# Performance work log

Measured on AMD Instinct MI355X. Metric: run time of the kernel, lower is better.

The kernel has to match this reference:

```python
import jax, jax.numpy as jnp
import numpy as np

B, S, T = 1024, 1024, 32  # batch, seq_len, num_tags


def setup_inputs() -> dict:
    key = jax.random.key(0)
    k1, k2, k3, k4 = jax.random.split(key, 4)
    logits = jax.random.normal(k1, (B, S, T), dtype=jnp.float32)
    transitions = jax.random.normal(k2, (T, T), dtype=jnp.float32)
    tags = jax.random.randint(k3, (B, S), 0, T)
    lengths = jax.random.randint(k4, (B,), 1, S + 1)
    return {"logits": logits, "transitions": transitions, "tags": tags, "lengths": lengths}


def _forward_alg(logits, transitions):
    # viterbi_0 = logits[:, 0, :]; then for t>=1:
    # v_next[b, j] = logsumexp_i(v[b, i] + trans[i, j]) + logits[b, t, j]
    v0 = logits[:, 0, :]  # (B, T)
    emits = jnp.swapaxes(logits[:, 1:, :], 0, 1)  # (S-1, B, T)

    def step(v, emit_t):
        v_next = jax.nn.logsumexp(v[:, :, None] + transitions[None, :, :], axis=1) + emit_t
        return v_next, None

    v_final, _ = jax.lax.scan(step, v0, emits)
    return jax.nn.logsumexp(v_final, axis=1)  # (B,)


def _score_sentence(logits, transitions, tags, lengths):
    # emission scores of gold tags, masked to t < length (note: original ignores
    # lengths in the forward algorithm but uses them here, faithfully reproduced)
    emit = jnp.take_along_axis(logits, tags[:, :, None], axis=2)[..., 0]  # (B, S)
    pos = jnp.arange(S)
    emit_mask = (pos[None, :] < lengths[:, None]).astype(logits.dtype)
    score = jnp.sum(emit * emit_mask, axis=1)
    # transition scores trans[tags[t-1], tags[t]] for 1 <= t < length
    trans_sc = transitions[tags[:, :-1], tags[:, 1:]]  # (B, S-1)
    trans_mask = (pos[None, 1:] < lengths[:, None]).astype(logits.dtype)
    score = score + jnp.sum(trans_sc * trans_mask, axis=1)
    return score  # (B,)


def reference(logits, transitions, tags, lengths):
    log_z = _forward_alg(logits, transitions)
    gold = _score_sentence(logits, transitions, tags, lengths)
    return jnp.mean(log_z - gold)
```

## Files before the change

### kernel.cpp

```cpp
#include <hip/hip_runtime.h>

#define NB 1024
#define NS 1024
#define NT 32
#define L2E 1.44269504088896340736f
#define LN2 0.69314718055994530942f

typedef short        bfrag  __attribute__((ext_vector_type(8)));
typedef float        cfrag  __attribute__((ext_vector_type(16)));
typedef __bf16       bf16x2 __attribute__((ext_vector_type(2)));
typedef float        f32x8  __attribute__((ext_vector_type(8)));
typedef float        f32x4  __attribute__((ext_vector_type(4)));
typedef float        f32x2  __attribute__((ext_vector_type(2)));
typedef unsigned int u32;
typedef unsigned int u32x4  __attribute__((ext_vector_type(4)));

__device__ __forceinline__ float fexp2(float x){ return __builtin_amdgcn_exp2f(x); }
__device__ __forceinline__ float flog2(float x){ return __builtin_amdgcn_logf(x); }

__device__ __forceinline__ u32 pkbf_rne(float a, float b){
    f32x2 t; t.x = a; t.y = b;
    return __builtin_bit_cast(u32, __builtin_convertvector(t, bf16x2));
}
__device__ __forceinline__ u32 pkbf_t(float a, float b){
    return __builtin_amdgcn_perm(__builtin_bit_cast(u32, b),
                                 __builtin_bit_cast(u32, a), 0x07060302u);
}
__device__ __forceinline__ bfrag mk_afrag(f32x8 v){
    u32x4 r;
    r[0] = pkbf_rne(v[0], v[1]); r[1] = pkbf_rne(v[2], v[3]);
    r[2] = pkbf_rne(v[4], v[5]); r[3] = pkbf_rne(v[6], v[7]);
    return __builtin_bit_cast(bfrag, r);
}
__device__ __forceinline__ int exref(float ref){
    u32 xb = __builtin_bit_cast(u32, ref);
    u32 xf = __builtin_amdgcn_readfirstlane(xb);
    int ex = (int)((xf >> 23) & 0xFFu) - 127;
    return ex < -120 ? -120 : (ex > 120 ? 120 : ex);
}

__device__ __forceinline__ int rho(int k){
    int bb = (k >> 2) & 3;
    return (bb == 1 || bb == 2) ? (k ^ 12) : k;
}

template<int N> struct ic { static constexpr int value = N; };
union accu { cfrag c; f32x2 p[8]; };
union q4u  { f32x4 v; f32x2 p[2]; };

__global__ __launch_bounds__(256, 8) void crf_chunk(
    const float* __restrict__ logits, const float* __restrict__ trans,
    const int* __restrict__ tags, const int* __restrict__ lens,
    u32* __restrict__ wmat, float* __restrict__ woff,
    float* __restrict__ gpart, float* __restrict__ outz)
{
    __shared__ __align__(16) float dscall[4 * 512];

    const int tid = threadIdx.x;
    const int wv  = tid >> 6, lt = tid & 63;
    const int m   = lt & 31,  h  = lt >> 5;
    const int bc  = blockIdx.x * 4 + wv;
    const int b   = bc >> 3,  c  = bc & 7;
    float* dsc = dscall + wv * 512;

    if (blockIdx.x == 0 && tid == 0) *outz = 0.0f;

    const float* base = logits + (size_t)b * NS * NT;
    const int    len  = lens[b];
    const int    tb   = b * NS;

    f32x8 Et0, Et1;
    #pragma unroll
    for (int j = 0; j < 8; j++){
        Et0[j] = fexp2(L2E * trans[rho(     8*h + j)*NT + m]);
        Et1[j] = fexp2(L2E * trans[rho(16 + 8*h + j)*NT + m]);
    }
    const bfrag A0f = mk_afrag(Et0);
    const bfrag A1f = mk_afrag(Et1);

    u32x4 B0v, B1v;
    #pragma unroll
    for (int d = 0; d < 4; d++){
        int k0 = 8*h + 2*d;      u32 v = 0;
        if (rho(k0)     == m) v |= 0x3F80u;
        if (rho(k0 + 1) == m) v |= 0x3F800000u;
        B0v[d] = v;
        int k1 = 16 + 8*h + 2*d; v = 0;
        if (rho(k1)     == m) v |= 0x3F80u;
        if (rho(k1 + 1) == m) v |= 0x3F800000u;
        B1v[d] = v;
    }

    cfrag zacc;
    #pragma unroll
    for (int q = 0; q < 16; q++) zacc[q] = 0.0f;

    int   offi = 0;
    float exf  = 0.0f;
    const int tbeg = c*128 + 1;

    float eA[4], eB[4];

    auto issue = [&](float (&e)[4], int k){
        const int t0 = tbeg + k*8 + 4*h;
        #pragma unroll
        for (int i = 0; i < 4; i++){
            int t = t0 + i; t = t > (NS-1) ? (NS-1) : t;
            e[i] = base[t*NT + m];
        }
    };
    auto commit = [&](float (&e)[4], int k){
        float* sp = dsc + (k & 1)*256 + (4*h)*32 + m;
        float a0 = (h == 0) ? -exf : 0.0f;
        sp[0]    = fexp2(fmaf(L2E, e[0], a0));
        sp[32]   = fexp2(L2E * e[1]);
        sp[64]   = fexp2(L2E * e[2]);
        sp[96]   = fexp2(L2E * e[3]);
    };

    auto procN = [&](int k, bool defer, auto nstc){
        constexpr int NST = decltype(nstc)::value;
        const float* db = dsc + (k & 1)*256 + 4*h;
        #pragma unroll
        for (int i = 0; i < NST; i++){
            accu acc;
            acc.c = __builtin_amdgcn_mfma_f32_32x32x16_bf16(
                        A0f, __builtin_bit_cast(bfrag, B0v), zacc, 0, 0, 0);
            acc.c = __builtin_amdgcn_mfma_f32_32x32x16_bf16(
                        A1f, __builtin_bit_cast(bfrag, B1v), acc.c, 0, 0, 0);

            q4u d0, d1, d2, d3;
            d0.v = *(const f32x4*)(db + i*32 +  0);
            d1.v = *(const f32x4*)(db + i*32 +  8);
            d2.v = *(const f32x4*)(db + i*32 + 16);
            d3.v = *(const f32x4*)(db + i*32 + 24);
            acc.p[0] *= d0.p[0]; acc.p[1] *= d0.p[1];
            acc.p[2] *= d1.p[0]; acc.p[3] *= d1.p[1];
            acc.p[4] *= d2.p[0]; acc.p[5] *= d2.p[1];
            acc.p[6] *= d3.p[0]; acc.p[7] *= d3.p[1];

            if (i == 3){
                int ex = exref(fmaxf(acc.c[0], acc.c[8]));
                offi += ex;
                f32x2 s2;
                s2.x = s2.y = __builtin_bit_cast(float, (u32)(127 - ex) << 23);
                #pragma unroll
                for (int q = 0; q < 8; q++) acc.p[q] *= s2;
            }
            if (i == 7 && defer){
                int ex = exref(fmaxf(acc.c[0], acc.c[8]));
                offi += ex;
                exf = (float)ex;
            }

            B0v[0] = pkbf_t(acc.c[0],  acc.c[1]);  B0v[1] = pkbf_t(acc.c[2],  acc.c[3]);
            B0v[2] = pkbf_t(acc.c[4],  acc.c[5]);  B0v[3] = pkbf_t(acc.c[6],  acc.c[7]);
            B1v[0] = pkbf_t(acc.c[8],  acc.c[9]);  B1v[1] = pkbf_t(acc.c[10], acc.c[11]);
            B1v[2] = pkbf_t(acc.c[12], acc.c[13]); B1v[3] = pkbf_t(acc.c[14], acc.c[15]);
        }
    };

    issue(eA, 0); commit(eA, 0);
    #pragma unroll 1
    for (int k = 0; k < 14; k += 2){
        issue(eB, k + 1);
        procN(k, true, ic<8>{});
        commit(eB, k + 1);
        issue(eA, k + 2);
        procN(k + 1, true, ic<8>{});
        commit(eA, k + 2);
    }
    issue(eB, 15);
    procN(14, true, ic<8>{});
    commit(eB, 15);
    if (c != 7) procN(15, false, ic<8>{});
    else        procN(15, false, ic<7>{});

    {
        u32* wp = wmat + (size_t)bc * 512 + (size_t)lt * 8;
        *(u32x4*)(wp)     = B0v;
        *(u32x4*)(wp + 4) = B1v;
    }
    if (lt == 0) woff[bc] = (float)offi;

    {
        const int t1 = tbeg + 2*lt;
        const int t2 = t1 + 1;
        const int i2 = t2 > (NS-1) ? (NS-1) : t2;
        const int g0 = tags[tb + t1 - 1];
        const int g1 = tags[tb + t1];
        const int g2 = tags[tb + i2];
        float gg = 0.0f;
        if (t1 < len) gg += base[t1*NT + g1] + trans[g0*NT + g1];
        if (t2 < len) gg += base[t2*NT + g2] + trans[g1*NT + g2];
        #pragma unroll
        for (int d = 1; d < 64; d <<= 1) gg += __shfl_xor(gg, d, 64);
        if (lt == 0){
            if (c == 0) gg += base[tags[tb]];
            gpart[bc] = gg;
        }
    }
}

__global__ __launch_bounds__(256) void crf_combine(
    const float* __restrict__ logits,
    const u32* __restrict__ wmat, const float* __restrict__ woff,
    const float* __restrict__ gpart, float* __restrict__ out)
{
    const int tid = threadIdx.x;
    const int wv  = tid >> 6, lt = tid & 63;
    const int m   = lt & 31,  h  = lt >> 5;
    const int b   = blockIdx.x * 4 + wv;
    const float* base = logits + (size_t)b * NS * NT;

    uint4 mf[16];
    const u32* wb = wmat + (size_t)b * 8 * 512 + (size_t)lt * 8;
    #pragma unroll
    for (int j = 0; j < 8; j++){
        mf[2*j]     = *(const uint4*)(wb + j*512);
        mf[2*j + 1] = *(const uint4*)(wb + j*512 + 4);
    }

    float4 gp0 = ((const float4*)(gpart + b*8))[0];
    float4 gp1 = ((const float4*)(gpart + b*8))[1];
    const float gold = (gp0.x + gp0.y) + (gp0.z + gp0.w)
                     + (gp1.x + gp1.y) + (gp1.z + gp1.w);

    float voff = 0.0f;
    #pragma unroll
    for (int cc = 0; cc < 8; cc++) voff += woff[b*8 + cc];

    u32x4 S0, S1;
    #pragma unroll
    for (int d = 0; d < 4; d++){
        int k0 = 8*h + 2*d;      u32 v = 0;
        if (rho(k0)     == m) v |= 0x3F80u;
        if (rho(k0 + 1) == m) v |= 0x3F800000u;
        S0[d] = v;
        int k1 = 16 + 8*h + 2*d; v = 0;
        if (rho(k1)     == m) v |= 0x3F80u;
        if (rho(k1 + 1) == m) v |= 0x3F800000u;
        S1[d] = v;
    }

    cfrag zacc;
    #pragma unroll
    for (int q = 0; q < 16; q++) zacc[q] = 0.0f;

    #pragma unroll
    for (int j = 7; j >= 0; j--){
        accu acc;
        acc.c = __builtin_amdgcn_mfma_f32_32x32x16_bf16(
                    __builtin_bit_cast(bfrag, mf[2*j]),
                    __builtin_bit_cast(bfrag, S0), zacc, 0, 0, 0);
        acc.c = __builtin_amdgcn_mfma_f32_32x32x16_bf16(
                    __builtin_bit_cast(bfrag, mf[2*j + 1]),
                    __builtin_bit_cast(bfrag, S1), acc.c, 0, 0, 0);

        float mx = acc.c[0];
        #pragma unroll
        for (int q = 1; q < 16; q++) mx = fmaxf(mx, acc.c[q]);
        #pragma unroll
        for (int d = 1; d < 64; d <<= 1) mx = fmaxf(mx, __shfl_xor(mx, d, 64));
        int ex = exref(mx);
        float sc = __builtin_bit_cast(float, (u32)(127 - ex) << 23);
        #pragma unroll
        for (int q = 0; q < 16; q++) acc.c[q] *= sc;
        voff += (float)ex;

        S0[0] = pkbf_t(acc.c[0],  acc.c[1]);  S0[1] = pkbf_t(acc.c[2],  acc.c[3]);
        S0[2] = pkbf_t(acc.c[4],  acc.c[5]);  S0[3] = pkbf_t(acc.c[6],  acc.c[7]);
        S1[0] = pkbf_t(acc.c[8],  acc.c[9]);  S1[1] = pkbf_t(acc.c[10], acc.c[11]);
        S1[2] = pkbf_t(acc.c[12], acc.c[13]); S1[3] = pkbf_t(acc.c[14], acc.c[15]);
    }

    u32x4 V0, V1;
    #pragma unroll
    for (int d = 0; d < 4; d++){
        int k0 = 8*h + 2*d;
        V0[d] = pkbf_rne(fexp2(L2E * base[rho(k0)]), fexp2(L2E * base[rho(k0+1)]));
        int k1 = 16 + 8*h + 2*d;
        V1[d] = pkbf_rne(fexp2(L2E * base[rho(k1)]), fexp2(L2E * base[rho(k1+1)]));
    }

    accu fin;
    fin.c = __builtin_amdgcn_mfma_f32_32x32x16_bf16(
                __builtin_bit_cast(bfrag, S0), __builtin_bit_cast(bfrag, V0),
                zacc, 0, 0, 0);
    fin.c = __builtin_amdgcn_mfma_f32_32x32x16_bf16(
                __builtin_bit_cast(bfrag, S1), __builtin_bit_cast(bfrag, V1),
                fin.c, 0, 0, 0);

    float s = 0.0f;
    #pragma unroll
    for (int q = 0; q < 16; q++) s += fin.c[q];
    s += __shfl_xor(s, 32, 64);

    if (lt == 0){
        float logz = LN2 * (voff + flog2(s));
        atomicAdd(out, (logz - gold) * (1.0f / (float)NB));
    }
}

extern "C" void kernel_launch(void* const* d_in, const int* in_sizes, int n_in,
                              void* d_out, int out_size, void* d_ws, size_t ws_size,
                              hipStream_t stream) {
    const float* logits = (const float*)d_in[0];
    const float* trans  = (const float*)d_in[1];
    const int*   tags   = (const int*)d_in[2];
    const int*   lens   = (const int*)d_in[3];

    u32*   wmat  = (u32*)d_ws;
    float* woff  = (float*)((char*)d_ws + 16u*1024u*1024u);
    float* gpart = woff + 8192;

    crf_chunk  <<<2048, 256, 0, stream>>>(logits, trans, tags, lens,
                                          wmat, woff, gpart, (float*)d_out);
    crf_combine<<< 256, 256, 0, stream>>>(logits, wmat, woff, gpart,
                                          (float*)d_out);
}
```

Before: 248.5 us.

## Split each wave's 128-step chunk into two interleaved 64-step sub-chains

Each wave now runs two independent transfer-matrix chains over the low and high halves of its 128-step chunk. Their MFMAs are interleaved so one chain's dependency latency is hidden behind the other's work, and the two products are merged at the end with two extra MFMA pairs and a rescale. This shortens the serial MFMA dependency chain per wave. The cost is doubled LDS per wave and more registers, so launch bounds drop from 8 to 4 blocks per SM, which lowers occupancy.

```diff
diff --git a/kernel.cpp b/kernel.cpp
--- a/kernel.cpp
+++ b/kernel.cpp
@@ -48,20 +48,24 @@
 union accu { cfrag c; f32x2 p[8]; };
 union q4u  { f32x4 v; f32x2 p[2]; };
 
-__global__ __launch_bounds__(256, 8) void crf_chunk(
+#define MFMA(A,B,C) __builtin_amdgcn_mfma_f32_32x32x16_bf16( \
+    (A), __builtin_bit_cast(bfrag, B), (C), 0, 0, 0)
+
+__global__ __launch_bounds__(256, 4) void crf_chunk(
     const float* __restrict__ logits, const float* __restrict__ trans,
     const int* __restrict__ tags, const int* __restrict__ lens,
     u32* __restrict__ wmat, float* __restrict__ woff,
     float* __restrict__ gpart, float* __restrict__ outz)
 {
-    __shared__ __align__(16) float dscall[4 * 512];
+    __shared__ __align__(16) float dscall[4 * 1024];
 
     const int tid = threadIdx.x;
     const int wv  = tid >> 6, lt = tid & 63;
     const int m   = lt & 31,  h  = lt >> 5;
     const int bc  = blockIdx.x * 4 + wv;
     const int b   = bc >> 3,  c  = bc & 7;
-    float* dsc = dscall + wv * 512;
+    float* dscL = dscall + wv * 1024;
+    float* dscH = dscL + 512;
 
     if (blockIdx.x == 0 && tid == 0) *outz = 0.0f;
 
@@ -78,30 +82,34 @@
     const bfrag A0f = mk_afrag(Et0);
     const bfrag A1f = mk_afrag(Et1);
 
-    u32x4 B0v, B1v;
+    u32x4 I0, I1;
     #pragma unroll
     for (int d = 0; d < 4; d++){
         int k0 = 8*h + 2*d;      u32 v = 0;
         if (rho(k0)     == m) v |= 0x3F80u;
         if (rho(k0 + 1) == m) v |= 0x3F800000u;
-        B0v[d] = v;
+        I0[d] = v;
         int k1 = 16 + 8*h + 2*d; v = 0;
         if (rho(k1)     == m) v |= 0x3F80u;
         if (rho(k1 + 1) == m) v |= 0x3F800000u;
-        B1v[d] = v;
-    }
+        I1[d] = v;
+    }
+
+    u32x4 L0 = I0, L1 = I1;
+    u32x4 H0 = I0, H1 = I1;
 
     cfrag zacc;
     #pragma unroll
     for (int q = 0; q < 16; q++) zacc[q] = 0.0f;
 
-    int   offi = 0;
-    float exf  = 0.0f;
-    const int tbeg = c*128 + 1;
-
-    float eA[4], eB[4];
-
-    auto issue = [&](float (&e)[4], int k){
+    int   offiL = 0,    offiH = 0;
+    float exfL  = 0.0f, exfH  = 0.0f;
+    const int tbegL = c*128 + 1;
+    const int tbegH = c*128 + 65;
+
+    float eLA[4], eLB[4], eHA[4], eHB[4];
+
+    auto issue = [&](float (&e)[4], int k, int tbeg){
         const int t0 = tbeg + k*8 + 4*h;
         #pragma unroll
         for (int i = 0; i < 4; i++){
@@ -109,7 +117,7 @@
             e[i] = base[t*NT + m];
         }
     };
-    auto commit = [&](float (&e)[4], int k){
+    auto commit = [&](float (&e)[4], int k, float* dsc, float exf){
         float* sp = dsc + (k & 1)*256 + (4*h)*32 + m;
         float a0 = (h == 0) ? -exf : 0.0f;
         sp[0]    = fexp2(fmaf(L2E, e[0], a0));
@@ -118,73 +126,134 @@
         sp[96]   = fexp2(L2E * e[3]);
     };
 
-    auto procN = [&](int k, bool defer, auto nstc){
-        constexpr int NST = decltype(nstc)::value;
-        const float* db = dsc + (k & 1)*256 + 4*h;
-        #pragma unroll
-        for (int i = 0; i < NST; i++){
-            accu acc;
-            acc.c = __builtin_amdgcn_mfma_f32_32x32x16_bf16(
-                        A0f, __builtin_bit_cast(bfrag, B0v), zacc, 0, 0, 0);
-            acc.c = __builtin_amdgcn_mfma_f32_32x32x16_bf16(
-                        A1f, __builtin_bit_cast(bfrag, B1v), acc.c, 0, 0, 0);
-
-            q4u d0, d1, d2, d3;
-            d0.v = *(const f32x4*)(db + i*32 +  0);
-            d1.v = *(const f32x4*)(db + i*32 +  8);
-            d2.v = *(const f32x4*)(db + i*32 + 16);
-            d3.v = *(const f32x4*)(db + i*32 + 24);
-            acc.p[0] *= d0.p[0]; acc.p[1] *= d0.p[1];
-            acc.p[2] *= d1.p[0]; acc.p[3] *= d1.p[1];
-            acc.p[4] *= d2.p[0]; acc.p[5] *= d2.p[1];
-            acc.p[6] *= d3.p[0]; acc.p[7] *= d3.p[1];
+    auto proc2 = [&](int k, bool defer, auto nhC){
+        constexpr int NH = decltype(nhC)::value;
+        const float* dbL = dscL + (k & 1)*256 + 4*h;
+        const float* dbH = dscH + (k & 1)*256 + 4*h;
+        #pragma unroll
+        for (int i = 0; i < 8; i++){
+            accu aL, aH;
+            aL.c = MFMA(A0f, L0, zacc);
+            if (i < NH) aH.c = MFMA(A0f, H0, zacc);
+            aL.c = MFMA(A1f, L1, aL.c);
+            if (i < NH) aH.c = MFMA(A1f, H1, aH.c);
+
+            {
+                q4u d0, d1, d2, d3;
+                d0.v = *(const f32x4*)(dbL + i*32 +  0);
+                d1.v = *(const f32x4*)(dbL + i*32 +  8);
+                d2.v = *(const f32x4*)(dbL + i*32 + 16);
+                d3.v = *(const f32x4*)(dbL + i*32 + 24);
+                aL.p[0] *= d0.p[0]; aL.p[1] *= d0.p[1];
+                aL.p[2] *= d1.p[0]; aL.p[3] *= d1.p[1];
+                aL.p[4] *= d2.p[0]; aL.p[5] *= d2.p[1];
+                aL.p[6] *= d3.p[0]; aL.p[7] *= d3.p[1];
+            }
+            if (i < NH){
+                q4u d0, d1, d2, d3;
+                d0.v = *(const f32x4*)(dbH + i*32 +  0);
+                d1.v = *(const f32x4*)(dbH + i*32 +  8);
+                d2.v = *(const f32x4*)(dbH + i*32 + 16);
+                d3.v = *(const f32x4*)(dbH + i*32 + 24);
+                aH.p[0] *= d0.p[0]; aH.p[1] *= d0.p[1];
+                aH.p[2] *= d1.p[0]; aH.p[3] *= d1.p[1];
+                aH.p[4] *= d2.p[0]; aH.p[5] *= d2.p[1];
+                aH.p[6] *= d3.p[0]; aH.p[7] *= d3.p[1];
+            }
 
             if (i == 3){
-                int ex = exref(fmaxf(acc.c[0], acc.c[8]));
-                offi += ex;
-                f32x2 s2;
-                s2.x = s2.y = __builtin_bit_cast(float, (u32)(127 - ex) << 23);
+                int exL = exref(fmaxf(aL.c[0], aL.c[8]));
+                offiL += exL;
+                f32x2 s2; s2.x = s2.y =
+                    __builtin_bit_cast(float, (u32)(127 - exL) << 23);
                 #pragma unroll
-                for (int q = 0; q < 8; q++) acc.p[q] *= s2;
+                for (int q = 0; q < 8; q++) aL.p[q] *= s2;
+                int exH = exref(fmaxf(aH.c[0], aH.c[8]));
+                offiH += exH;
+                f32x2 s3; s3.x = s3.y =
+                    __builtin_bit_cast(float, (u32)(127 - exH) << 23);
+                #pragma unroll
+                for (int q = 0; q < 8; q++) aH.p[q] *= s3;
             }
             if (i == 7 && defer){
-                int ex = exref(fmaxf(acc.c[0], acc.c[8]));
-                offi += ex;
-                exf = (float)ex;
-            }
-
-            B0v[0] = pkbf_t(acc.c[0],  acc.c[1]);  B0v[1] = pkbf_t(acc.c[2],  acc.c[3]);
-            B0v[2] = pkbf_t(acc.c[4],  acc.c[5]);  B0v[3] = pkbf_t(acc.c[6],  acc.c[7]);
-            B1v[0] = pkbf_t(acc.c[8],  acc.c[9]);  B1v[1] = pkbf_t(acc.c[10], acc.c[11]);
-            B1v[2] = pkbf_t(acc.c[12], acc.c[13]); B1v[3] = pkbf_t(acc.c[14], acc.c[15]);
+                int exL = exref(fmaxf(aL.c[0], aL.c[8]));
+                offiL += exL; exfL = (float)exL;
+                int exH = exref(fmaxf(aH.c[0], aH.c[8]));
+                offiH += exH; exfH = (float)exH;
+            }
+
+            L0[0] = pkbf_t(aL.c[0],  aL.c[1]);  L0[1] = pkbf_t(aL.c[2],  aL.c[3]);
+            L0[2] = pkbf_t(aL.c[4],  aL.c[5]);  L0[3] = pkbf_t(aL.c[6],  aL.c[7]);
+            L1[0] = pkbf_t(aL.c[8],  aL.c[9]);  L1[1] = pkbf_t(aL.c[10], aL.c[11]);
+            L1[2] = pkbf_t(aL.c[12], aL.c[13]); L1[3] = pkbf_t(aL.c[14], aL.c[15]);
+            if (i < NH){
+                H0[0] = pkbf_t(aH.c[0],  aH.c[1]);  H0[1] = pkbf_t(aH.c[2],  aH.c[3]);
+                H0[2] = pkbf_t(aH.c[4],  aH.c[5]);  H0[3] = pkbf_t(aH.c[6],  aH.c[7]);
+                H1[0] = pkbf_t(aH.c[8],  aH.c[9]);  H1[1] = pkbf_t(aH.c[10], aH.c[11]);
+                H1[2] = pkbf_t(aH.c[12], aH.c[13]); H1[3] = pkbf_t(aH.c[14], aH.c[15]);
+            }
         }
     };
 
-    issue(eA, 0); commit(eA, 0);
+    issue(eLA, 0, tbegL); issue(eHA, 0, tbegH);
+    commit(eLA, 0, dscL, 0.0f); commit(eHA, 0, dscH, 0.0f);
     #pragma unroll 1
-    for (int k = 0; k < 14; k += 2){
-        issue(eB, k + 1);
-        procN(k, true, ic<8>{});
-        commit(eB, k + 1);
-        issue(eA, k + 2);
-        procN(k + 1, true, ic<8>{});
-        commit(eA, k + 2);
-    }
-    issue(eB, 15);
-    procN(14, true, ic<8>{});
-    commit(eB, 15);
-    if (c != 7) procN(15, false, ic<8>{});
-    else        procN(15, false, ic<7>{});
+    for (int k = 0; k < 6; k += 2){
+        issue(eLB, k + 1, tbegL); issue(eHB, k + 1, tbegH);
+        proc2(k, true, ic<8>{});
+        commit(eLB, k + 1, dscL, exfL); commit(eHB, k + 1, dscH, exfH);
+        issue(eLA, k + 2, tbegL); issue(eHA, k + 2, tbegH);
+        proc2(k + 1, true, ic<8>{});
+        commit(eLA, k + 2, dscL, exfL); commit(eHA, k + 2, dscH, exfH);
+    }
+    issue(eLB, 7, tbegL); issue(eHB, 7, tbegH);
+    proc2(6, true, ic<8>{});
+    commit(eLB, 7, dscL, exfL); commit(eHB, 7, dscH, exfH);
+    if (c != 7) proc2(7, false, ic<8>{});
+    else        proc2(7, false, ic<7>{});
+
+    u32x4 F0, F1;
+    int offi;
+    {
+        accu tt;
+        tt.c = MFMA(__builtin_bit_cast(bfrag, H0), I0, zacc);
+        tt.c = MFMA(__builtin_bit_cast(bfrag, H1), I1, tt.c);
+        u32x4 G0, G1;
+        G0[0] = pkbf_t(tt.c[0],  tt.c[1]);  G0[1] = pkbf_t(tt.c[2],  tt.c[3]);
+        G0[2] = pkbf_t(tt.c[4],  tt.c[5]);  G0[3] = pkbf_t(tt.c[6],  tt.c[7]);
+        G1[0] = pkbf_t(tt.c[8],  tt.c[9]);  G1[1] = pkbf_t(tt.c[10], tt.c[11]);
+        G1[2] = pkbf_t(tt.c[12], tt.c[13]); G1[3] = pkbf_t(tt.c[14], tt.c[15]);
+
+        accu zz;
+        zz.c = MFMA(__builtin_bit_cast(bfrag, G0), L0, zacc);
+        zz.c = MFMA(__builtin_bit_cast(bfrag, G1), L1, zz.c);
+
+        float mx = zz.c[0];
+        #pragma unroll
+        for (int q = 1; q < 16; q++) mx = fmaxf(mx, zz.c[q]);
+        #pragma unroll
+        for (int d = 1; d < 64; d <<= 1) mx = fmaxf(mx, __shfl_xor(mx, d, 64));
+        int ex = exref(mx);
+        float sc = __builtin_bit_cast(float, (u32)(127 - ex) << 23);
+        #pragma unroll
+        for (int q = 0; q < 16; q++) zz.c[q] *= sc;
+        offi = offiL + offiH + ex;
+
+        F0[0] = pkbf_t(zz.c[0],  zz.c[1]);  F0[1] = pkbf_t(zz.c[2],  zz.c[3]);
+        F0[2] = pkbf_t(zz.c[4],  zz.c[5]);  F0[3] = pkbf_t(zz.c[6],  zz.c[7]);
+        F1[0] = pkbf_t(zz.c[8],  zz.c[9]);  F1[1] = pkbf_t(zz.c[10], zz.c[11]);
+        F1[2] = pkbf_t(zz.c[12], zz.c[13]); F1[3] = pkbf_t(zz.c[14], zz.c[15]);
+    }
 
     {
         u32* wp = wmat + (size_t)bc * 512 + (size_t)lt * 8;
-        *(u32x4*)(wp)     = B0v;
-        *(u32x4*)(wp + 4) = B1v;
+        *(u32x4*)(wp)     = F0;
+        *(u32x4*)(wp + 4) = F1;
     }
     if (lt == 0) woff[bc] = (float)offi;
 
     {
-        const int t1 = tbeg + 2*lt;
+        const int t1 = tbegL + 2*lt;
         const int t2 = t1 + 1;
         const int i2 = t2 > (NS-1) ? (NS-1) : t2;
         const int g0 = tags[tb + t1 - 1];
@@ -250,12 +319,8 @@
     #pragma unroll
     for (int j = 7; j >= 0; j--){
         accu acc;
-        acc.c = __builtin_amdgcn_mfma_f32_32x32x16_bf16(
-                    __builtin_bit_cast(bfrag, mf[2*j]),
-                    __builtin_bit_cast(bfrag, S0), zacc, 0, 0, 0);
-        acc.c = __builtin_amdgcn_mfma_f32_32x32x16_bf16(
-                    __builtin_bit_cast(bfrag, mf[2*j + 1]),
-                    __builtin_bit_cast(bfrag, S1), acc.c, 0, 0, 0);
+        acc.c = MFMA(__builtin_bit_cast(bfrag, mf[2*j]),     S0, zacc);
+        acc.c = MFMA(__builtin_bit_cast(bfrag, mf[2*j + 1]), S1, acc.c);
 
         float mx = acc.c[0];
         #pragma unroll
@@ -284,12 +349,8 @@
     }
 
     accu fin;
-    fin.c = __builtin_amdgcn_mfma_f32_32x32x16_bf16(
-                __builtin_bit_cast(bfrag, S0), __builtin_bit_cast(bfrag, V0),
-                zacc, 0, 0, 0);
-    fin.c = __builtin_amdgcn_mfma_f32_32x32x16_bf16(
-                __builtin_bit_cast(bfrag, S1), __builtin_bit_cast(bfrag, V1),
-                fin.c, 0, 0, 0);
+    fin.c = MFMA(__builtin_bit_cast(bfrag, S0), V0, zacc);
+    fin.c = MFMA(__builtin_bit_cast(bfrag, S1), V1, fin.c);
 
     float s = 0.0f;
     #pragma unroll
```

New measurement: 248.3 us. No clear change (-0.0%).
